# Optimization experiments

Measured on AMD Instinct MI355X. Metric: run time of the kernel, lower is better.

## Reference

```python
import jax, jax.numpy as jnp
import numpy as np
from jax import lax

EMBED = 64
FRAMES = 3
NNB = FRAMES - 1  # neighbor frames


def conv3x3(x, w, b):
    # x: [B,Cin,H,W], w: [Cout,Cin,3,3]
    y = lax.conv_general_dilated(x, w, (1, 1), [(1, 1), (1, 1)],
                                 dimension_numbers=("NCHW", "OIHW", "NCHW"))
    return y + b[None, :, None, None]


def setup_inputs() -> dict:
    key = jax.random.key(0)
    ks = jax.random.split(key, 9)
    s = lambda *sh: 1.0 / np.sqrt(np.prod(sh[1:]))
    return {
        "neighbor_frames": jax.random.normal(ks[0], (2, NNB, 96, 96), jnp.float32),
        "enc_w1": jax.random.normal(ks[1], (EMBED, 1, 3, 3), jnp.float32) * s(EMBED, 1, 3, 3),
        "enc_b1": jnp.zeros((EMBED,), jnp.float32),
        "enc_w2": jax.random.normal(ks[2], (EMBED, EMBED, 3, 3), jnp.float32) * s(EMBED, EMBED, 3, 3),
        "enc_b2": jnp.zeros((EMBED,), jnp.float32),
        "q_w": jax.random.normal(ks[3], (EMBED, NNB * EMBED), jnp.float32) * s(EMBED, NNB * EMBED),
        "q_b": jnp.zeros((EMBED,), jnp.float32),
        "k_w": jax.random.normal(ks[4], (EMBED, NNB * EMBED), jnp.float32) * s(EMBED, NNB * EMBED),
        "k_b": jnp.zeros((EMBED,), jnp.float32),
        "v_w": jax.random.normal(ks[5], (EMBED, NNB * EMBED), jnp.float32) * s(EMBED, NNB * EMBED),
        "v_b": jnp.zeros((EMBED,), jnp.float32),
    }


def reference(neighbor_frames, enc_w1, enc_b1, enc_w2, enc_b2,
              q_w, q_b, k_w, k_b, v_w, v_b):
    B, N, H, W = neighbor_frames.shape
    x = neighbor_frames.reshape(B * N, 1, H, W)
    # conv encoder (3x3 -> relu -> 3x3 -> relu)
    f = jax.nn.relu(conv3x3(x, enc_w1, enc_b1))
    f = jax.nn.relu(conv3x3(f, enc_w2, enc_b2))
    C = f.shape[1]
    # [B,N,C,H,W] -> [B, C*N? no: permute(0,2,1,3,4) -> B, C, N, H, W -> B, C*N, H, W]
    feat = f.reshape(B, N, C, H, W).transpose(0, 2, 1, 3, 4).reshape(B, C * N, H, W)
    # 1x1 qkv convs == per-pixel linear; flatten spatial to tokens t = H*W
    feat_t = feat.reshape(B, C * N, H * W)  # [B, Cin, T]
    Q = jnp.einsum("oc,bct->bot", q_w, feat_t) + q_b[None, :, None]
    K = jnp.einsum("oc,bct->bot", k_w, feat_t) + k_b[None, :, None]
    V = jnp.einsum("oc,bct->bot", v_w, feat_t) + v_b[None, :, None]
    scale = 1.0 / jnp.sqrt(jnp.asarray(Q.shape[1], Q.dtype))
    attn = jnp.einsum("bcn,bcm->bnm", Q, K) * scale  # [B, T, T]
    attn = jax.nn.softmax(attn, axis=-1)
    ctx = jnp.einsum("bnm,bcm->bcn", attn, V)  # [B, C, T]
    return ctx.reshape(B, C, H, W)
```

## Files before the change

kernel.cpp:

```cpp
#include <hip/hip_runtime.h>
#include <hip/hip_bf16.h>

#define TOK 9216
#define KSPLIT 5

typedef _Float16 half8 __attribute__((ext_vector_type(8)));
typedef float f32x4 __attribute__((ext_vector_type(4)));

#define GLOAD_LDS(g, l) \
    __builtin_amdgcn_global_load_lds((const __attribute__((address_space(1))) void*)(g), \
                                     (__attribute__((address_space(3))) void*)(l), 16, 0, 0)

#define QSCALE 0.18033688011112042f

#define OFF_F1   0u
#define SZ_F1    (4u*64u*TOK)
#define OFF_FEAT (OFF_F1 + SZ_F1)
#define SZ_FEAT  (2u*128u*TOK)
#define OFF_W1   (OFF_FEAT + SZ_FEAT + 3u*2u*64u*TOK)
#define OFF_B1   (OFF_W1 + 576u)
#define OFF_W2T  (OFF_B1 + 64u)
#define OFF_B2   (OFF_W2T + 36864u)
#define OFF_WCAT (OFF_B2 + 64u)
#define OFF_BCAT (OFF_WCAT + 24576u)

#define OFF_QT   OFF_F1
#define OFF_KT   (OFF_F1 + 589824u)
#define OFF_VH   (OFF_F1 + 1179648u)

#define OFF_SLAB0 1769472u
#define OFF_ML2   (OFF_FEAT + 9u*589824u)

__device__ __forceinline__ const float* part_base_c(const float* ws, int slab) {
    return ws + (slab == 0 ? OFF_SLAB0 : (OFF_FEAT + (unsigned)(slab - 1) * 589824u));
}
__device__ __forceinline__ float* part_base(float* ws, int slab) {
    return ws + (slab == 0 ? OFF_SLAB0 : (OFF_FEAT + (unsigned)(slab - 1) * 589824u));
}

__global__ __launch_bounds__(256) void conv1_kernel(
    const float* __restrict__ x,
    const float* __restrict__ w1, const float* __restrict__ b1,
    const float* __restrict__ w2, const float* __restrict__ b2,
    const float* __restrict__ qw, const float* __restrict__ qb,
    const float* __restrict__ kw, const float* __restrict__ kb,
    const float* __restrict__ vw, const float* __restrict__ vb,
    float* __restrict__ ws)
{
    int gid = blockIdx.x * 256 + threadIdx.x;

    if (gid < 64) ws[OFF_B2 + gid] = b2[gid];
    if (gid < 36864) {
        int co = gid / 576; int rem = gid % 576;
        int ci = rem / 9;  int tp = rem % 9;
        ((_Float16*)(ws + OFF_W2T))[co*576 + tp*64 + ci] = (_Float16)w2[gid];
    }
    if (gid < 24576) {
        int o = gid >> 7; int kidx = gid & 127;
        int n = kidx >> 6, c = kidx & 63;
        int sc = c*2 + n;
        float v;
        if (o < 64)       v = qw[o*128 + sc] * QSCALE;
        else if (o < 128) v = kw[(o-64)*128 + sc];
        else              v = vw[(o-128)*128 + sc];
        ((_Float16*)(ws + OFF_WCAT))[gid] = (_Float16)v;
    }
    if (gid < 192) {
        float v;
        if (gid < 64)       v = qb[gid] * QSCALE;
        else if (gid < 128) v = kb[gid-64];
        else                v = vb[gid-128];
        ws[OFF_BCAT + gid] = v;
    }

    _Float16* f1h = (_Float16*)(ws + OFF_F1);
    int img = gid / TOK;
    int p   = gid % TOK;
    int h = p / 96, w = p % 96;
    float xv[9];
    #pragma unroll
    for (int dh = 0; dh < 3; ++dh)
        #pragma unroll
        for (int dw = 0; dw < 3; ++dw) {
            int r = h + dh - 1, c = w + dw - 1;
            bool ok = (r >= 0) && (r < 96) && (c >= 0) && (c < 96);
            xv[dh*3 + dw] = ok ? x[img*TOK + r*96 + c] : 0.f;
        }
    _Float16* dst = f1h + (size_t)gid * 64;
    #pragma unroll
    for (int g8 = 0; g8 < 8; ++g8) {
        union { _Float16 h[8]; uint4 u; } pk8;
        #pragma unroll
        for (int j = 0; j < 8; ++j) {
            int co = g8*8 + j;
            float a = b1[co];
            #pragma unroll
            for (int t = 0; t < 9; ++t) a += w1[co*9 + t] * xv[t];
            pk8.h[j] = (_Float16)fmaxf(a, 0.f);
        }
        *(uint4*)&dst[g8*8] = pk8.u;
    }
}

__global__ __launch_bounds__(256) void conv2_kernel(float* __restrict__ ws)
{
    int bid = blockIdx.x;
    int img = bid & 3;
    int tile = bid >> 2;
    int tid = threadIdx.x;
    int lane = tid & 63, w = tid >> 6;
    int lr = lane & 15, lk = lane >> 4;

    const _Float16* f1h = (const _Float16*)(ws + OFF_F1) + (size_t)img*TOK*64;
    const _Float16* Wc  = (const _Float16*)(ws + OFF_W2T);
    const float* b2f = ws + OFF_B2;

    int t = tile*64 + w*16 + lr;
    int h = t / 96, wc = t % 96;

    half8 z8;
    #pragma unroll
    for (int i = 0; i < 8; ++i) z8[i] = (_Float16)0.f;

    f32x4 acc[4];
    #pragma unroll
    for (int cs = 0; cs < 4; ++cs) {
        float bv = b2f[cs*16 + lr];
        acc[cs] = (f32x4){bv, bv, bv, bv};
    }

    #pragma unroll
    for (int ch = 0; ch < 18; ++ch) {
        int k = ch*32 + lk*8;
        int tap = k >> 6, ci = k & 63;
        int dh = tap / 3, dw = tap % 3;
        int r = h + dh - 1, c = wc + dw - 1;
        half8 af = z8;
        if ((unsigned)r < 96u && (unsigned)c < 96u)
            af = *(const half8*)&f1h[(size_t)(r*96 + c)*64 + ci];
        #pragma unroll
        for (int cs = 0; cs < 4; ++cs) {
            half8 bfr = *(const half8*)&Wc[(size_t)(cs*16 + lr)*576 + k];
            acc[cs] = __builtin_amdgcn_mfma_f32_16x16x32_f16(af, bfr, acc[cs], 0, 0, 0);
        }
    }

    _Float16* featH2 = (_Float16*)(ws + OFF_FEAT) + (size_t)img*TOK*64;
    int tbase = tile*64 + w*16 + 4*lk;
    #pragma unroll
    for (int cs = 0; cs < 4; ++cs)
        #pragma unroll
        for (int r = 0; r < 4; ++r)
            featH2[(size_t)(tbase + r)*64 + cs*16 + lr] = (_Float16)fmaxf(acc[cs][r], 0.f);
}

__global__ __launch_bounds__(256) void qkvgemm_kernel(float* __restrict__ ws)
{
    int bid = blockIdx.x;
    int b   = bid / 288;
    int tt0 = (bid % 288) * 32;
    int tid = threadIdx.x;
    int lane = tid & 63, w = tid >> 6;
    int lr = lane & 15, lk = lane >> 4;

    const _Float16* fH = (const _Float16*)(ws + OFF_FEAT) + (size_t)b*2*TOK*64;
    const _Float16* W  = (const _Float16*)(ws + OFF_WCAT);
    const float* bc = ws + OFF_BCAT;
    _Float16* QT = (_Float16*)(ws + OFF_QT) + (size_t)b*TOK*64;
    _Float16* KT = (_Float16*)(ws + OFF_KT) + (size_t)b*TOK*64;
    _Float16* VH = (_Float16*)(ws + OFF_VH) + (size_t)b*64*TOK;

    half8 bf[2][4];
    #pragma unroll
    for (int tt = 0; tt < 2; ++tt)
        #pragma unroll
        for (int kc = 0; kc < 4; ++kc) {
            int k = kc*32 + lk*8;
            bf[tt][kc] = *(const half8*)&fH[(size_t)(k >> 6)*TOK*64
                                            + (size_t)(tt0 + tt*16 + lr)*64 + (k & 63)];
        }

    half8 af[3][4];
    #pragma unroll
    for (int i = 0; i < 3; ++i)
        #pragma unroll
        for (int kc = 0; kc < 4; ++kc)
            af[i][kc] = *(const half8*)&W[(size_t)((w*3 + i)*16 + lr)*128 + kc*32 + lk*8];

    #pragma unroll
    for (int i = 0; i < 3; ++i) {
        int ot = w*3 + i;
        f32x4 a0, a1;
        #pragma unroll
        for (int r = 0; r < 4; ++r) {
            float bv = bc[ot*16 + 4*lk + r];
            a0[r] = bv; a1[r] = bv;
        }
        #pragma unroll
        for (int kc = 0; kc < 4; ++kc) {
            a0 = __builtin_amdgcn_mfma_f32_16x16x32_f16(af[i][kc], bf[0][kc], a0, 0, 0, 0);
            a1 = __builtin_amdgcn_mfma_f32_16x16x32_f16(af[i][kc], bf[1][kc], a1, 0, 0, 0);
        }
        #pragma unroll
        for (int tt = 0; tt < 2; ++tt) {
            f32x4 a = tt ? a1 : a0;
            int t = tt0 + tt*16 + lr;
            if (ot < 4) {
                union { _Float16 h[4]; uint2 u; } p;
                #pragma unroll
                for (int r = 0; r < 4; ++r) p.h[r] = (_Float16)a[r];
                *(uint2*)&QT[(size_t)t*64 + ot*16 + 4*lk] = p.u;
            } else if (ot < 8) {
                union { _Float16 h[4]; uint2 u; } p;
                #pragma unroll
                for (int r = 0; r < 4; ++r) p.h[r] = (_Float16)a[r];
                *(uint2*)&KT[(size_t)t*64 + (ot-4)*16 + 4*lk] = p.u;
            } else {
                #pragma unroll
                for (int r = 0; r < 4; ++r)
                    VH[(size_t)((ot-8)*16 + 4*lk + r)*TOK + t] = (_Float16)a[r];
            }
        }
    }
}

__global__ __launch_bounds__(512, 6) void attn_kernel(float* __restrict__ ws)
{
    __shared__ __align__(16) char smem[32768];
    float* ldsf = (float*)smem;

    int bid = blockIdx.x;
    int b   = bid / (72*KSPLIT);
    int rem = bid % (72*KSPLIT);
    int qt  = rem / KSPLIT;
    int ks  = rem % KSPLIT;
    int tid = threadIdx.x;
    int lane = tid & 63, w = tid >> 6;
    int wq = w & 3;
    int q0 = qt * 128;
    int lr = lane & 15;
    int lk = lane >> 4;

    int kb0 = (ks*144)/KSPLIT, kb1 = ((ks+1)*144)/KSPLIT;
    int nit = kb1 - kb0;
    int slab = b*KSPLIT + ks;

    const _Float16* Qt = (const _Float16*)(ws + OFF_QT) + (size_t)b*TOK*64;
    const _Float16* Kt = (const _Float16*)(ws + OFF_KT) + (size_t)b*TOK*64;
    const _Float16* Vh = (const _Float16*)(ws + OFF_VH) + (size_t)b*64*TOK;
    float* part = part_base(ws, slab);
    float* ml   = ws + OFF_ML2 + (size_t)slab*2*TOK;

    half8 qB[2];
    #pragma unroll
    for (int ch = 0; ch < 2; ++ch)
        qB[ch] = *(const half8*)&Qt[(size_t)(q0 + w*16 + lr)*64 + ch*32 + lk*8];

    const f32x4 Z4 = (f32x4){0.f, 0.f, 0.f, 0.f};
    half8 ones;
    #pragma unroll
    for (int i = 0; i < 8; ++i) ones[i] = (_Float16)1.0f;

    f32x4 O[4];
    #pragma unroll
    for (int cs = 0; cs < 4; ++cs) O[cs] = Z4;
    f32x4 lacc = Z4;
    float mM = -INFINITY;

    int segl = ((lane & 7) ^ ((lane >> 3) & 7)) * 8;
    int rrow = w*8 + (lane >> 3);
    unsigned kOff = (unsigned)(kb0*64 + rrow)*64u + (unsigned)segl;
    unsigned vOff = (unsigned)rrow*(unsigned)TOK + (unsigned)(kb0*64) + (unsigned)segl;
    unsigned wbase = (unsigned)(w * 1024);

    GLOAD_LDS(Kt + kOff, smem +         wbase);
    GLOAD_LDS(Vh + vOff, smem + 16384 + wbase);
    asm volatile("s_waitcnt vmcnt(0)" ::: "memory");
    __builtin_amdgcn_s_barrier();

    for (int it = 0; it < nit; ++it) {
        char* sKb = smem +         (it & 1) * 8192;
        char* sVb = smem + 16384 + (it & 1) * 8192;

        if (it + 1 < nit) {
            unsigned bufo = (unsigned)(((it + 1) & 1) * 8192) + wbase;
            GLOAD_LDS(Kt + kOff + (unsigned)(it + 1) * 4096u, smem + bufo);
            GLOAD_LDS(Vh + vOff + (unsigned)(it + 1) * 64u,   smem + 16384 + bufo);
        }

        f32x4 S[4];
        __builtin_amdgcn_s_setprio(1);
        #pragma unroll
        for (int st = 0; st < 4; ++st) {
            int t = st*16 + lr;
            half8 kA0 = *(const half8*)(sKb + ((t*128 +      lk*16) ^ ((t&7)<<4)));
            half8 kA1 = *(const half8*)(sKb + ((t*128 + 64 + lk*16) ^ ((t&7)<<4)));
            f32x4 s = __builtin_amdgcn_mfma_f32_16x16x32_f16(kA0, qB[0], Z4, 0, 0, 0);
            S[st]   = __builtin_amdgcn_mfma_f32_16x16x32_f16(kA1, qB[1], s,  0, 0, 0);
        }
        __builtin_amdgcn_s_setprio(0);

        float a0 = fmaxf(fmaxf(S[0][0], S[0][1]), S[0][2]);
        float a1 = fmaxf(fmaxf(S[0][3], S[1][0]), S[1][1]);
        float a2 = fmaxf(fmaxf(S[1][2], S[1][3]), S[2][0]);
        float a3 = fmaxf(fmaxf(S[2][1], S[2][2]), S[2][3]);
        float a4 = fmaxf(fmaxf(S[3][0], S[3][1]), S[3][2]);
        float pm = fmaxf(fmaxf(fmaxf(a0, a1), a2),
                         fmaxf(fmaxf(a3, a4), S[3][3]));
        pm = fmaxf(pm, __shfl_xor(pm, 16));
        pm = fmaxf(pm, __shfl_xor(pm, 32));

        if (__any(pm > mM + 8.0f)) {
            float mn = fmaxf(mM, pm);
            float fs = exp2f(mM - mn);
            mM = mn;
            #pragma unroll
            for (int cs = 0; cs < 4; ++cs)
                #pragma unroll
                for (int r = 0; r < 4; ++r) O[cs][r] *= fs;
            #pragma unroll
            for (int r = 0; r < 4; ++r) lacc[r] *= fs;
        }

        #pragma unroll
        for (int st = 0; st < 4; ++st)
            #pragma unroll
            for (int r = 0; r < 4; ++r)
                S[st][r] = exp2f(S[st][r] - mM);

        unsigned int pk2[4][2];
        #pragma unroll
        for (int st = 0; st < 4; ++st) {
            pk2[st][0] = __builtin_bit_cast(unsigned int,
                             __builtin_amdgcn_cvt_pkrtz(S[st][0], S[st][1]));
            pk2[st][1] = __builtin_bit_cast(unsigned int,
                             __builtin_amdgcn_cvt_pkrtz(S[st][2], S[st][3]));
        }

        int srcA = lr + 32*(lk & 1);
        int sel  = lk >> 1;
        __builtin_amdgcn_s_setprio(1);
        #pragma unroll
        for (int ch2 = 0; ch2 < 2; ++ch2) {
            union { unsigned int u[4]; half8 h; } pb;
            #pragma unroll
            for (int w2 = 0; w2 < 4; ++w2) {
                int src = srcA + 16*(w2 >> 1);
                int lo = __shfl((int)pk2[ch2*2 + 0][w2 & 1], src);
                int hi = __shfl((int)pk2[ch2*2 + 1][w2 & 1], src);
                pb.u[w2] = (unsigned int)(sel ? hi : lo);
            }
            lacc = __builtin_amdgcn_mfma_f32_16x16x32_f16(ones, pb.h, lacc, 0, 0, 0);
            #pragma unroll
            for (int cs = 0; cs < 4; ++cs) {
                int crow = cs*16 + lr;
                half8 vA = *(const half8*)(sVb + ((crow*128 + ch2*64 + lk*16) ^ ((crow&7)<<4)));
                O[cs] = __builtin_amdgcn_mfma_f32_16x16x32_f16(vA, pb.h, O[cs], 0, 0, 0);
            }
        }
        __builtin_amdgcn_s_setprio(0);

        asm volatile("s_waitcnt vmcnt(0)" ::: "memory");
        __builtin_amdgcn_s_barrier();
    }

    if (lk == 0) {
        ml[q0 + w*16 + lr]       = mM;
        ml[TOK + q0 + w*16 + lr] = lacc[0];
    }

    #pragma unroll
    for (int h = 0; h < 2; ++h) {
        if ((w >> 2) == h) {
            #pragma unroll
            for (int cs = 0; cs < 4; ++cs)
                #pragma unroll
                for (int r = 0; r < 4; ++r)
                    ldsf[(cs*16 + 4*lk + r)*68 + wq*16 + lr] = O[cs][r];
        }
        __syncthreads();
        int c = tid >> 3, qs = (tid & 7) * 8;
        const float* srcr = &ldsf[c*68 + qs];
        float* dstr = &part[(size_t)c*TOK + q0 + h*64 + qs];
        *(float4*)&dstr[0] = *(const float4*)&srcr[0];
        *(float4*)&dstr[4] = *(const float4*)&srcr[4];
        __syncthreads();
    }
}

__global__ __launch_bounds__(256) void recombine_kernel(
    const float* __restrict__ ws, float* __restrict__ out)
{
    int gid = blockIdx.x * 256 + threadIdx.x;
    int b   = gid / 9216;
    int rem = gid % 9216;
    int cg  = rem / 2304;
    int t   = (rem % 2304) * 4;
    const float* mlp = ws + OFF_ML2;

    float4 m4[KSPLIT], l4[KSPLIT];
    float4 M = {-INFINITY, -INFINITY, -INFINITY, -INFINITY};
    #pragma unroll
    for (int ks = 0; ks < KSPLIT; ++ks) {
        int slab = b*KSPLIT + ks;
        m4[ks] = *(const float4*)&mlp[(size_t)slab*2*TOK + t];
        l4[ks] = *(const float4*)&mlp[(size_t)slab*2*TOK + TOK + t];
        M.x = fmaxf(M.x, m4[ks].x); M.y = fmaxf(M.y, m4[ks].y);
        M.z = fmaxf(M.z, m4[ks].z); M.w = fmaxf(M.w, m4[ks].w);
    }
    float4 wgt[KSPLIT];
    float4 den = {0.f, 0.f, 0.f, 0.f};
    #pragma unroll
    for (int ks = 0; ks < KSPLIT; ++ks) {
        wgt[ks].x = exp2f(m4[ks].x - M.x); wgt[ks].y = exp2f(m4[ks].y - M.y);
        wgt[ks].z = exp2f(m4[ks].z - M.z); wgt[ks].w = exp2f(m4[ks].w - M.w);
        den.x += l4[ks].x * wgt[ks].x; den.y += l4[ks].y * wgt[ks].y;
        den.z += l4[ks].z * wgt[ks].z; den.w += l4[ks].w * wgt[ks].w;
    }
    float4 inv = {1.f/den.x, 1.f/den.y, 1.f/den.z, 1.f/den.w};
    #pragma unroll
    for (int cc = 0; cc < 16; ++cc) {
        int c = cg*16 + cc;
        float4 acc = {0.f, 0.f, 0.f, 0.f};
        #pragma unroll
        for (int ks = 0; ks < KSPLIT; ++ks) {
            const float* part = part_base_c(ws, b*KSPLIT + ks);
            float4 p4 = *(const float4*)&part[(size_t)c*TOK + t];
            acc.x += p4.x * wgt[ks].x; acc.y += p4.y * wgt[ks].y;
            acc.z += p4.z * wgt[ks].z; acc.w += p4.w * wgt[ks].w;
        }
        float4 o4 = {acc.x*inv.x, acc.y*inv.y, acc.z*inv.z, acc.w*inv.w};
        *(float4*)&out[(size_t)(b*64 + c)*TOK + t] = o4;
    }
}

extern "C" void kernel_launch(void* const* d_in, const int* in_sizes, int n_in,
                              void* d_out, int out_size, void* d_ws, size_t ws_size,
                              hipStream_t stream)
{
    const float* frames = (const float*)d_in[0];
    const float* w1 = (const float*)d_in[1];
    const float* b1 = (const float*)d_in[2];
    const float* w2 = (const float*)d_in[3];
    const float* b2 = (const float*)d_in[4];
    const float* qw = (const float*)d_in[5];
    const float* qb = (const float*)d_in[6];
    const float* kw = (const float*)d_in[7];
    const float* kb = (const float*)d_in[8];
    const float* vw = (const float*)d_in[9];
    const float* vb = (const float*)d_in[10];
    float* ws = (float*)d_ws;
    float* out = (float*)d_out;

    hipLaunchKernelGGL(conv1_kernel, dim3(144), dim3(256), 0, stream,
                       frames, w1, b1, w2, b2, qw, qb, kw, kb, vw, vb, ws);
    hipLaunchKernelGGL(conv2_kernel, dim3(576), dim3(256), 0, stream, ws);
    hipLaunchKernelGGL(qkvgemm_kernel, dim3(576), dim3(256), 0, stream, ws);
    hipLaunchKernelGGL(attn_kernel, dim3(2*72*KSPLIT), dim3(512), 0, stream, ws);
    hipLaunchKernelGGL(recombine_kernel, dim3(72), dim3(256), 0, stream, ws, out);
}
```

Before: 157.4 us.

## Fuse conv2 with QKV projection via LDS tile and widen conv1/recombine grids

Merges the conv2 and QKV GEMM kernels into one kernel. Each block computes conv2 for both neighbor frames of a 64-token tile, stores the fp16 features in a swizzled LDS tile, and runs the QKV MFMA directly from LDS, so the feature tensor no longer round-trips through global memory and one launch is dropped. The workspace layout is reorganised so that Q/K/V and the partial slabs fit the new regions. conv1 now splits each pixel's output channels across two threads, and recombine uses four times as many blocks, both to raise parallelism. The fused kernel has fewer blocks than the old conv2 (288 vs 576) and does more work per block, which may reduce occupancy and latency hiding.

```diff
diff --git a/kernel.cpp b/kernel.cpp
--- a/kernel.cpp
+++ b/kernel.cpp
@@ -24,18 +24,19 @@
 #define OFF_WCAT (OFF_B2 + 64u)
 #define OFF_BCAT (OFF_WCAT + 24576u)
 
-#define OFF_QT   OFF_F1
-#define OFF_KT   (OFF_F1 + 589824u)
-#define OFF_VH   (OFF_F1 + 1179648u)
-
-#define OFF_SLAB0 1769472u
-#define OFF_ML2   (OFF_FEAT + 9u*589824u)
+#define OFF_QT   4718592u
+#define OFF_KT   5308416u
+#define OFF_VH   5898240u
+
+#define OFF_ML2  (OFF_FEAT + 9u*589824u)
 
 __device__ __forceinline__ const float* part_base_c(const float* ws, int slab) {
-    return ws + (slab == 0 ? OFF_SLAB0 : (OFF_FEAT + (unsigned)(slab - 1) * 589824u));
+    return ws + (slab < 8 ? (unsigned)slab * 589824u
+                          : 6488064u + (unsigned)(slab - 8) * 589824u);
 }
 __device__ __forceinline__ float* part_base(float* ws, int slab) {
-    return ws + (slab == 0 ? OFF_SLAB0 : (OFF_FEAT + (unsigned)(slab - 1) * 589824u));
+    return ws + (slab < 8 ? (unsigned)slab * 589824u
+                          : 6488064u + (unsigned)(slab - 8) * 589824u);
 }
 
 __global__ __launch_bounds__(256) void conv1_kernel(
@@ -74,8 +75,9 @@
     }
 
     _Float16* f1h = (_Float16*)(ws + OFF_F1);
-    int img = gid / TOK;
-    int p   = gid % TOK;
+    int px = gid >> 1, half = gid & 1;
+    int img = px / TOK;
+    int p   = px % TOK;
     int h = p / 96, w = p % 96;
     float xv[9];
     #pragma unroll
@@ -86,13 +88,13 @@
             bool ok = (r >= 0) && (r < 96) && (c >= 0) && (c < 96);
             xv[dh*3 + dw] = ok ? x[img*TOK + r*96 + c] : 0.f;
         }
-    _Float16* dst = f1h + (size_t)gid * 64;
-    #pragma unroll
-    for (int g8 = 0; g8 < 8; ++g8) {
+    _Float16* dst = f1h + (size_t)px * 64 + half * 32;
+    #pragma unroll
+    for (int g8 = 0; g8 < 4; ++g8) {
         union { _Float16 h[8]; uint4 u; } pk8;
         #pragma unroll
         for (int j = 0; j < 8; ++j) {
-            int co = g8*8 + j;
+            int co = half*32 + g8*8 + j;
             float a = b1[co];
             #pragma unroll
             for (int t = 0; t < 9; ++t) a += w1[co*9 + t] * xv[t];
@@ -102,16 +104,17 @@
     }
 }
 
-__global__ __launch_bounds__(256) void conv2_kernel(float* __restrict__ ws)
+__global__ __launch_bounds__(256) void conv2qkv_kernel(float* __restrict__ ws)
 {
+    __shared__ __align__(16) char fT[16384];
+
     int bid = blockIdx.x;
-    int img = bid & 3;
-    int tile = bid >> 2;
+    int b   = bid / 144;
+    int tile = bid % 144;
     int tid = threadIdx.x;
     int lane = tid & 63, w = tid >> 6;
     int lr = lane & 15, lk = lane >> 4;
 
-    const _Float16* f1h = (const _Float16*)(ws + OFF_F1) + (size_t)img*TOK*64;
     const _Float16* Wc  = (const _Float16*)(ws + OFF_W2T);
     const float* b2f = ws + OFF_B2;
 
@@ -122,103 +125,96 @@
     #pragma unroll
     for (int i = 0; i < 8; ++i) z8[i] = (_Float16)0.f;
 
-    f32x4 acc[4];
-    #pragma unroll
-    for (int cs = 0; cs < 4; ++cs) {
-        float bv = b2f[cs*16 + lr];
-        acc[cs] = (f32x4){bv, bv, bv, bv};
-    }
-
-    #pragma unroll
-    for (int ch = 0; ch < 18; ++ch) {
-        int k = ch*32 + lk*8;
-        int tap = k >> 6, ci = k & 63;
-        int dh = tap / 3, dw = tap % 3;
-        int r = h + dh - 1, c = wc + dw - 1;
-        half8 af = z8;
-        if ((unsigned)r < 96u && (unsigned)c < 96u)
-            af = *(const half8*)&f1h[(size_t)(r*96 + c)*64 + ci];
+    #pragma unroll
+    for (int n = 0; n < 2; ++n) {
+        const _Float16* f1h = (const _Float16*)(ws + OFF_F1) + (size_t)(b*2 + n)*TOK*64;
+        f32x4 acc[4];
         #pragma unroll
         for (int cs = 0; cs < 4; ++cs) {
-            half8 bfr = *(const half8*)&Wc[(size_t)(cs*16 + lr)*576 + k];
-            acc[cs] = __builtin_amdgcn_mfma_f32_16x16x32_f16(af, bfr, acc[cs], 0, 0, 0);
-        }
-    }
-
-    _Float16* featH2 = (_Float16*)(ws + OFF_FEAT) + (size_t)img*TOK*64;
-    int tbase = tile*64 + w*16 + 4*lk;
-    #pragma unroll
-    for (int cs = 0; cs < 4; ++cs)
-        #pragma unroll
-        for (int r = 0; r < 4; ++r)
-            featH2[(size_t)(tbase + r)*64 + cs*16 + lr] = (_Float16)fmaxf(acc[cs][r], 0.f);
-}
-
-__global__ __launch_bounds__(256) void qkvgemm_kernel(float* __restrict__ ws)
-{
-    int bid = blockIdx.x;
-    int b   = bid / 288;
-    int tt0 = (bid % 288) * 32;
-    int tid = threadIdx.x;
-    int lane = tid & 63, w = tid >> 6;
-    int lr = lane & 15, lk = lane >> 4;
-
-    const _Float16* fH = (const _Float16*)(ws + OFF_FEAT) + (size_t)b*2*TOK*64;
+            float bv = b2f[cs*16 + lr];
+            acc[cs] = (f32x4){bv, bv, bv, bv};
+        }
+        #pragma unroll
+        for (int ch = 0; ch < 18; ++ch) {
+            int k = ch*32 + lk*8;
+            int tap = k >> 6, ci = k & 63;
+            int dh = tap / 3, dw = tap % 3;
+            int r = h + dh - 1, c = wc + dw - 1;
+            half8 af = z8;
+            if ((unsigned)r < 96u && (unsigned)c < 96u)
+                af = *(const half8*)&f1h[(size_t)(r*96 + c)*64 + ci];
+            #pragma unroll
+            for (int cs = 0; cs < 4; ++cs) {
+                half8 bfr = *(const half8*)&Wc[(size_t)(cs*16 + lr)*576 + k];
+                acc[cs] = __builtin_amdgcn_mfma_f32_16x16x32_f16(af, bfr, acc[cs], 0, 0, 0);
+            }
+        }
+        #pragma unroll
+        for (int cs = 0; cs < 4; ++cs)
+            #pragma unroll
+            for (int r = 0; r < 4; ++r) {
+                int tl = w*16 + 4*lk + r;
+                int off = tl*256 + (n*64 + cs*16 + lr)*2;
+                *(_Float16*)(fT + (off ^ ((tl&7)<<4))) =
+                    (_Float16)fmaxf(acc[cs][r], 0.f);
+            }
+    }
+    __syncthreads();
+
     const _Float16* W  = (const _Float16*)(ws + OFF_WCAT);
     const float* bc = ws + OFF_BCAT;
     _Float16* QT = (_Float16*)(ws + OFF_QT) + (size_t)b*TOK*64;
     _Float16* KT = (_Float16*)(ws + OFF_KT) + (size_t)b*TOK*64;
     _Float16* VH = (_Float16*)(ws + OFF_VH) + (size_t)b*64*TOK;
 
-    half8 bf[2][4];
-    #pragma unroll
-    for (int tt = 0; tt < 2; ++tt)
+    half8 bf[4][4];
+    #pragma unroll
+    for (int tt = 0; tt < 4; ++tt)
         #pragma unroll
         for (int kc = 0; kc < 4; ++kc) {
-            int k = kc*32 + lk*8;
-            bf[tt][kc] = *(const half8*)&fH[(size_t)(k >> 6)*TOK*64
-                                            + (size_t)(tt0 + tt*16 + lr)*64 + (k & 63)];
-        }
-
-    half8 af[3][4];
+            int tl = tt*16 + lr;
+            bf[tt][kc] = *(const half8*)(fT + ((tl*256 + kc*64 + lk*16) ^ ((tl&7)<<4)));
+        }
+
+    half8 af3[3][4];
     #pragma unroll
     for (int i = 0; i < 3; ++i)
         #pragma unroll
         for (int kc = 0; kc < 4; ++kc)
-            af[i][kc] = *(const half8*)&W[(size_t)((w*3 + i)*16 + lr)*128 + kc*32 + lk*8];
+            af3[i][kc] = *(const half8*)&W[(size_t)((w*3 + i)*16 + lr)*128 + kc*32 + lk*8];
 
     #pragma unroll
     for (int i = 0; i < 3; ++i) {
         int ot = w*3 + i;
-        f32x4 a0, a1;
+        f32x4 a[4];
         #pragma unroll
         for (int r = 0; r < 4; ++r) {
             float bv = bc[ot*16 + 4*lk + r];
-            a0[r] = bv; a1[r] = bv;
-        }
-        #pragma unroll
-        for (int kc = 0; kc < 4; ++kc) {
-            a0 = __builtin_amdgcn_mfma_f32_16x16x32_f16(af[i][kc], bf[0][kc], a0, 0, 0, 0);
-            a1 = __builtin_amdgcn_mfma_f32_16x16x32_f16(af[i][kc], bf[1][kc], a1, 0, 0, 0);
-        }
-        #pragma unroll
-        for (int tt = 0; tt < 2; ++tt) {
-            f32x4 a = tt ? a1 : a0;
-            int t = tt0 + tt*16 + lr;
+            #pragma unroll
+            for (int tt = 0; tt < 4; ++tt) a[tt][r] = bv;
+        }
+        #pragma unroll
+        for (int kc = 0; kc < 4; ++kc)
+            #pragma unroll
+            for (int tt = 0; tt < 4; ++tt)
+                a[tt] = __builtin_amdgcn_mfma_f32_16x16x32_f16(af3[i][kc], bf[tt][kc], a[tt], 0, 0, 0);
+        #pragma unroll
+        for (int tt = 0; tt < 4; ++tt) {
+            int tg = tile*64 + tt*16 + lr;
             if (ot < 4) {
                 union { _Float16 h[4]; uint2 u; } p;
                 #pragma unroll
-                for (int r = 0; r < 4; ++r) p.h[r] = (_Float16)a[r];
-                *(uint2*)&QT[(size_t)t*64 + ot*16 + 4*lk] = p.u;
+                for (int r = 0; r < 4; ++r) p.h[r] = (_Float16)a[tt][r];
+                *(uint2*)&QT[(size_t)tg*64 + ot*16 + 4*lk] = p.u;
             } else if (ot < 8) {
                 union { _Float16 h[4]; uint2 u; } p;
                 #pragma unroll
-                for (int r = 0; r < 4; ++r) p.h[r] = (_Float16)a[r];
-                *(uint2*)&KT[(size_t)t*64 + (ot-4)*16 + 4*lk] = p.u;
+                for (int r = 0; r < 4; ++r) p.h[r] = (_Float16)a[tt][r];
+                *(uint2*)&KT[(size_t)tg*64 + (ot-4)*16 + 4*lk] = p.u;
             } else {
                 #pragma unroll
                 for (int r = 0; r < 4; ++r)
-                    VH[(size_t)((ot-8)*16 + 4*lk + r)*TOK + t] = (_Float16)a[r];
+                    VH[(size_t)((ot-8)*16 + 4*lk + r)*TOK + tg] = (_Float16)a[tt][r];
             }
         }
     }
@@ -391,11 +387,11 @@
 __global__ __launch_bounds__(256) void recombine_kernel(
     const float* __restrict__ ws, float* __restrict__ out)
 {
-    int gid = blockIdx.x * 256 + threadIdx.x;
-    int b   = gid / 9216;
-    int rem = gid % 9216;
-    int cg  = rem / 2304;
-    int t   = (rem % 2304) * 4;
+    int bid = blockIdx.x;
+    int b   = bid / 144;
+    int g2  = (bid % 144) * 256 + threadIdx.x;
+    int cq  = g2 / 2304;
+    int t   = (g2 % 2304) * 4;
     const float* mlp = ws + OFF_ML2;
 
     float4 m4[KSPLIT], l4[KSPLIT];
@@ -419,8 +415,8 @@
     }
     float4 inv = {1.f/den.x, 1.f/den.y, 1.f/den.z, 1.f/den.w};
     #pragma unroll
-    for (int cc = 0; cc < 16; ++cc) {
-        int c = cg*16 + cc;
+    for (int cc = 0; cc < 4; ++cc) {
+        int c = cq*4 + cc;
         float4 acc = {0.f, 0.f, 0.f, 0.f};
         #pragma unroll
         for (int ks = 0; ks < KSPLIT; ++ks) {
@@ -452,10 +448,9 @@
     float* ws = (float*)d_ws;
     float* out = (float*)d_out;
 
-    hipLaunchKernelGGL(conv1_kernel, dim3(144), dim3(256), 0, stream,
+    hipLaunchKernelGGL(conv1_kernel, dim3(288), dim3(256), 0, stream,
                        frames, w1, b1, w2, b2, qw, qb, kw, kb, vw, vb, ws);
-    hipLaunchKernelGGL(conv2_kernel, dim3(576), dim3(256), 0, stream, ws);
-    hipLaunchKernelGGL(qkvgemm_kernel, dim3(576), dim3(256), 0, stream, ws);
+    hipLaunchKernelGGL(conv2qkv_kernel, dim3(288), dim3(256), 0, stream, ws);
     hipLaunchKernelGGL(attn_kernel, dim3(2*72*KSPLIT), dim3(512), 0, stream, ws);
-    hipLaunchKernelGGL(recombine_kernel, dim3(72), dim3(256), 0, stream, ws, out);
-}
+    hipLaunchKernelGGL(recombine_kernel, dim3(288), dim3(256), 0, stream, ws, out);
+}
```

After: 156.9 us, median of 2. About the same (-0.3%).
